# Kernel tuning notes

Measured on AMD Instinct MI355X. Metric: run time of the kernel, lower is better.

## Reference

```python
import jax, jax.numpy as jnp
import numpy as np

COUNT = 8  # hardcoded 8x8 patch grid in the original module


def setup_inputs() -> dict:
    key = jax.random.key(0)
    kx, = jax.random.split(key, 1)
    x = jax.random.normal(kx, (8, 64, 512, 512), dtype=jnp.float32)
    gamma = jnp.zeros((1,), dtype=jnp.float32)  # nn.Parameter(torch.zeros(1))
    return {"x": x, "gamma": gamma}


def reference(x, gamma):
    B, C, H, W = x.shape
    s = H // COUNT  # stride; original uses height-derived stride for both dims
    # Extract the 8x8 grid of patches without loops:
    # (B,C,H,W) -> (B,C,cnt,s,cnt,s) -> (B,cnt,cnt,C,s,s) -> (B,P,C,s*s)
    p = x.reshape(B, C, COUNT, s, COUNT, s)
    p = p.transpose(0, 2, 4, 1, 3, 5).reshape(B, COUNT * COUNT, C, s * s)
    # channel-channel energy per patch: [B,P,C,C]
    energy = jnp.einsum('bpci,bpdi->bpcd', p, p)
    # DANet trick: max - energy, then softmax over last dim
    energy_new = jnp.max(energy, axis=-1, keepdims=True) - energy
    attention = jax.nn.softmax(energy_new, axis=-1)
    out = jnp.einsum('bpcd,bpdi->bpci', attention, p)
    # reassemble spatial map
    out = out.reshape(B, COUNT, COUNT, C, s, s)
    out = out.transpose(0, 3, 1, 4, 2, 5).reshape(B, C, H, W)
    # NOTE: in the torch code y = x is an alias and x is overwritten in-place,
    # so the final result is gamma * attended + attended.
    return gamma[0] * out + out
```

## Files before the change

### kernel.cpp

```cpp
#include <hip/hip_runtime.h>


#define NW  512
#define HWs 262144

typedef __attribute__((ext_vector_type(4)))  __bf16 bf4;
typedef __attribute__((ext_vector_type(8)))  __bf16 bf8;
typedef __attribute__((ext_vector_type(16))) float  f32x16;

#define MFMA __builtin_amdgcn_mfma_f32_32x32x16_bf16
#define F4E(v,j) ((j)==0?(v).x:(j)==1?(v).y:(j)==2?(v).z:(v).w)

__device__ __forceinline__ void bar_lgkm() {
  asm volatile("s_waitcnt lgkmcnt(0)" ::: "memory");
  __builtin_amdgcn_s_barrier();
}

__device__ __forceinline__ int soff(int c, int rb) {
  return c * 1024 + (rb & 512) + ((rb & 511) ^ ((c & 31) << 4));
}

extern "C" __global__ __launch_bounds__(512, 2)
void k1_gram(const float* __restrict__ x, float* __restrict__ ep) {
  __shared__ char lds[133120];
  char* sHi = lds;
  char* sLo = lds + 65536;
  float* S_lds = (float*)lds;

  const int t   = threadIdx.x;
  const int w8  = t >> 6;
  const int l   = t & 63;
  const int l31 = l & 31, hh = l >> 5;
  const int pc  = w8;
  const int cld = t >> 7;
  const int hf  = (t >> 6) & 1;

  const int bid = blockIdx.x;
  const int b  = bid >> 5;
  const int pr = (bid >> 2) & 7;
  const int hq = bid & 3;
  const float* xb = x + (size_t)b * 64 * HWs + (size_t)(pr * 64 + hq * 16) * NW
                  + hf * 256 + l * 4;

  f32x16 aG00, aG01, aG10, aG11, aS00, aS01, aS10, aS11;
#pragma unroll
  for (int i = 0; i < 16; ++i) {
    aG00[i]=0.f; aG01[i]=0.f; aG10[i]=0.f; aG11[i]=0.f;
    aS00[i]=0.f; aS01[i]=0.f; aS10[i]=0.f; aS11[i]=0.f;
  }

  float4 ra[16];
#pragma unroll
  for (int j = 0; j < 16; ++j)
    ra[j] = *(const float4*)(xb + (size_t)(j * 4 + cld) * HWs);

  for (int r = 0; r < 16; ++r) {
#pragma unroll
    for (int j = 0; j < 16; ++j) {
      const int c = j * 4 + cld;
      const float4 v = ra[j];
      bf4 h, lo;
      h[0]=(__bf16)v.x; h[1]=(__bf16)v.y; h[2]=(__bf16)v.z; h[3]=(__bf16)v.w;
      lo[0]=(__bf16)(v.x-(float)h[0]); lo[1]=(__bf16)(v.y-(float)h[1]);
      lo[2]=(__bf16)(v.z-(float)h[2]); lo[3]=(__bf16)(v.w-(float)h[3]);
      const int wb = c * 1024 + hf * 512 + ((l * 8) ^ ((c & 31) << 4));
      *(bf4*)(sHi + wb) = h;
      *(bf4*)(sLo + wb) = lo;
    }
    if (r + 1 < 16) {
#pragma unroll
      for (int j = 0; j < 16; ++j)
        ra[j] = *(const float4*)(xb + (size_t)(j * 4 + cld) * HWs
                                 + (size_t)(r + 1) * NW);
    }
    bar_lgkm();
#pragma unroll
    for (int ks = 0; ks < 4; ++ks) {
      const int rb = pc * 128 + ks * 32 + hh * 16;
      const bf8 a0 = *(const bf8*)(sHi + soff(l31, rb));
      const bf8 a1 = *(const bf8*)(sHi + soff(32 + l31, rb));
      const bf8 q0 = *(const bf8*)(sLo + soff(l31, rb));
      const bf8 q1 = *(const bf8*)(sLo + soff(32 + l31, rb));
      aG00 = MFMA(a0, a0, aG00, 0, 0, 0);
      aG01 = MFMA(a0, a1, aG01, 0, 0, 0);
      aG10 = MFMA(a1, a0, aG10, 0, 0, 0);
      aG11 = MFMA(a1, a1, aG11, 0, 0, 0);
      aS00 = MFMA(a0, q0, aS00, 0, 0, 0);
      aS01 = MFMA(a0, q1, aS01, 0, 0, 0);
      aS10 = MFMA(a1, q0, aS10, 0, 0, 0);
      aS11 = MFMA(a1, q1, aS11, 0, 0, 0);
    }
    bar_lgkm();
  }

#pragma unroll
  for (int i = 0; i < 16; ++i) {
    const int rr = (i & 3) + ((i >> 2) << 3) + (hh << 2);
    S_lds[pc * 4160 + (rr)      * 65 + l31]      = aS00[i];
    S_lds[pc * 4160 + (rr)      * 65 + 32 + l31] = aS01[i];
    S_lds[pc * 4160 + (32 + rr) * 65 + l31]      = aS10[i];
    S_lds[pc * 4160 + (32 + rr) * 65 + 32 + l31] = aS11[i];
  }
  bar_lgkm();
  const int pat = b * 64 + pr * 8 + pc;
  float* epb = ep + ((size_t)(pat * 4 + hq) << 12);
#pragma unroll
  for (int i = 0; i < 16; ++i) {
    const int rr = (i & 3) + ((i >> 2) << 3) + (hh << 2);
    epb[(rr)      * 64 + l31]      = aG00[i] + aS00[i] + S_lds[pc*4160 + (l31)    *65 + rr];
    epb[(rr)      * 64 + 32 + l31] = aG01[i] + aS01[i] + S_lds[pc*4160 + (32+l31) *65 + rr];
    epb[(32 + rr) * 64 + l31]      = aG10[i] + aS10[i] + S_lds[pc*4160 + (l31)    *65 + 32 + rr];
    epb[(32 + rr) * 64 + 32 + l31] = aG11[i] + aS11[i] + S_lds[pc*4160 + (32+l31) *65 + 32 + rr];
  }
}

extern "C" __global__ __launch_bounds__(256)
void k2_softmax(const float* __restrict__ ep, const float* __restrict__ g,
                __bf16* __restrict__ attn) {
  const int pat = blockIdx.x;
  const int w4 = threadIdx.x >> 6, l = threadIdx.x & 63;
  const float gs = 1.0f + g[0];
  const float* e0 = ep + ((size_t)(pat * 4) << 12);
#pragma unroll 1
  for (int cc = 0; cc < 16; ++cc) {
    const int c = w4 * 16 + cc;
    const int o = c * 64 + l;
    const float e = e0[o] + e0[4096 + o] + e0[8192 + o] + e0[12288 + o];
    float mn = e;
#pragma unroll
    for (int off = 32; off; off >>= 1) mn = fminf(mn, __shfl_xor(mn, off));
    const float w = __expf(mn - e);
    float s = w;
#pragma unroll
    for (int off = 32; off; off >>= 1) s += __shfl_xor(s, off);
    attn[(size_t)pat * 4096 + o] = (__bf16)(gs * w / s);
  }
}

extern "C" __global__ __launch_bounds__(512, 2)
void k3_pv(const float* __restrict__ x, const __bf16* __restrict__ attn,
           float* __restrict__ out) {
  __shared__ char lds[139264];
  char* nat = lds;
  char* pT  = lds + 65536;

  const int t   = threadIdx.x;
  const int w8  = t >> 6;
  const int l   = t & 63;
  const int l31 = l & 31, hh = l >> 5;
  const int pc  = w8;
  const int cld = t >> 7;
  const int hf  = (t >> 6) & 1;
  const int cb  = t & 15;
  const int wb0 = t >> 4;

  const int bid = blockIdx.x;
  const int b  = bid >> 5;
  const int pr = (bid >> 2) & 7;
  const int hq = bid & 3;
  const float* xb = x + (size_t)b * 64 * HWs + (size_t)(pr * 64 + hq * 16) * NW
                  + hf * 256 + l * 4;
  float* ob = out + (size_t)b * 64 * HWs + (size_t)(pr * 64 + hq * 16) * NW;
  const int pat = b * 64 + pr * 8 + pc;

  bf8 af0[4], af1[4];
#pragma unroll
  for (int ks = 0; ks < 4; ++ks) {
    af0[ks] = *(const bf8*)(attn + (size_t)pat * 4096 + (l31)      * 64 + ks * 16 + hh * 8);
    af1[ks] = *(const bf8*)(attn + (size_t)pat * 4096 + (32 + l31) * 64 + ks * 16 + hh * 8);
  }

  float4 ra[16];
#pragma unroll
  for (int j = 0; j < 16; ++j)
    ra[j] = *(const float4*)(xb + (size_t)(j * 4 + cld) * HWs);

  for (int r = 0; r < 16; ++r) {
#pragma unroll
    for (int j = 0; j < 16; ++j) {
      const int c = j * 4 + cld;
      const float4 v = ra[j];
      bf4 h;
      h[0]=(__bf16)v.x; h[1]=(__bf16)v.y; h[2]=(__bf16)v.z; h[3]=(__bf16)v.w;
      *(bf4*)(nat + c * 1024 + hf * 512 + ((l * 8) ^ ((c & 31) << 4))) = h;
    }
    if (r + 1 < 16) {
#pragma unroll
      for (int j = 0; j < 16; ++j)
        ra[j] = *(const float4*)(xb + (size_t)(j * 4 + cld) * HWs
                                 + (size_t)(r + 1) * NW);
    }
    bar_lgkm();
#pragma unroll
    for (int kk = 0; kk < 4; ++kk) {
      const int w0 = (wb0 + kk * 32) * 4;
      bf4 rd0, rd1, rd2, rd3;
      {
        const int c0 = cb * 4;
        const int hfb = (w0 >> 8) * 512;
        const int ib2 = (w0 & 255) * 2;
        rd0 = *(const bf4*)(nat + (c0    ) * 1024 + hfb + (ib2 ^ (((c0    ) & 31) << 4)));
        rd1 = *(const bf4*)(nat + (c0 + 1) * 1024 + hfb + (ib2 ^ (((c0 + 1) & 31) << 4)));
        rd2 = *(const bf4*)(nat + (c0 + 2) * 1024 + hfb + (ib2 ^ (((c0 + 2) & 31) << 4)));
        rd3 = *(const bf4*)(nat + (c0 + 3) * 1024 + hfb + (ib2 ^ (((c0 + 3) & 31) << 4)));
      }
#pragma unroll
      for (int jj = 0; jj < 4; ++jj) {
        bf4 wv;
        wv[0] = rd0[jj]; wv[1] = rd1[jj]; wv[2] = rd2[jj]; wv[3] = rd3[jj];
        *(bf4*)(pT + (size_t)(w0 + jj) * 144 + cb * 8) = wv;
      }
    }
    bar_lgkm();
#pragma unroll
    for (int ib = 0; ib < 2; ++ib) {
      f32x16 o0, o1;
#pragma unroll
      for (int i = 0; i < 16; ++i) { o0[i] = 0.f; o1[i] = 0.f; }
      const char* prow = pT + (size_t)(pc * 64 + ib * 32 + l31) * 144;
#pragma unroll
      for (int ks = 0; ks < 4; ++ks) {
        const bf8 pa = *(const bf8*)(prow + ks * 32 + hh * 16);
        o0 = MFMA(pa, af0[ks], o0, 0, 0, 0);
        o1 = MFMA(pa, af1[ks], o1, 0, 0, 0);
      }
#pragma unroll
      for (int rq = 0; rq < 4; ++rq) {
        const int wloc = pc * 64 + ib * 32 + rq * 8 + hh * 4;
        float* orow = ob + (size_t)r * NW + wloc;
        float4 q0; q0.x=o0[rq*4+0]; q0.y=o0[rq*4+1]; q0.z=o0[rq*4+2]; q0.w=o0[rq*4+3];
        *(float4*)(orow + (size_t)l31 * HWs) = q0;
        float4 q1; q1.x=o1[rq*4+0]; q1.y=o1[rq*4+1]; q1.z=o1[rq*4+2]; q1.w=o1[rq*4+3];
        *(float4*)(orow + (size_t)(32 + l31) * HWs) = q1;
      }
    }
    bar_lgkm();
  }
}

#define NS1 16
#define NS3 16

__device__ __forceinline__ void fb_load1(const float* g1, int st, float4 (&R)[16]) {
  const float* gp = g1 + (size_t)st * 4 * NW;
#pragma unroll
  for (int rl = 0; rl < 4; ++rl)
#pragma unroll
    for (int j = 0; j < 4; ++j)
      R[rl * 4 + j] = *(const float4*)(gp + (size_t)rl * NW + j * 4);
}
__device__ __forceinline__ void fb_cvtw1(char* wH, char* wL, int q_ld, int swzw,
                                         const float4 (&R)[16]) {
#pragma unroll
  for (int rl = 0; rl < 4; ++rl)
#pragma unroll
    for (int s = 0; s < 2; ++s) {
      const float4 va = R[rl * 4 + s * 2], vb = R[rl * 4 + s * 2 + 1];
      const float f[8] = {va.x, va.y, va.z, va.w, vb.x, vb.y, vb.z, vb.w};
      bf8 h, lo;
#pragma unroll
      for (int e = 0; e < 8; ++e) { h[e] = (__bf16)f[e]; lo[e] = (__bf16)(f[e] - (float)h[e]); }
      const int boff = (rl * 128 + q_ld * 32 + s * 16) ^ swzw;
      *(bf8*)(wH + boff) = h;
      *(bf8*)(wL + boff) = lo;
    }
}
__device__ __forceinline__ void fb_load3(const float* g3, int st, float4 (&R)[16]) {
  const float* gp = g3 + (size_t)st * 4 * NW;
#pragma unroll
  for (int cc = 0; cc < 4; ++cc)
#pragma unroll
    for (int j = 0; j < 4; ++j)
      R[cc * 4 + j] = *(const float4*)(gp + (size_t)cc * HWs + j * 4);
}
__device__ __forceinline__ void fb_cvtw3(char* sT, int cg, int iq, const float4 (&R)[16]) {
#pragma unroll
  for (int w = 0; w < 16; ++w) {
    bf4 q;
#pragma unroll
    for (int cc = 0; cc < 4; ++cc) q[cc] = (__bf16)F4E(R[cc * 4 + (w >> 2)], w & 3);
    const int iloc = iq * 16 + w;
    const int sw = ((iloc & 15) ^ ((iloc >> 4) & 7)) << 4;
    const int boff = (iloc & 127) * 256 + ((((iloc >> 7) << 7) + cg * 8) ^ sw);
    *(bf4*)(sT + boff) = q;
  }
}
extern "C" __global__ __launch_bounds__(256, 2)
void spectralAgg_fallback(const float* __restrict__ x, const float* __restrict__ g,
                          float* __restrict__ out) {
  __shared__ char lds[73728];
  char* sH = lds;
  char* sL = lds + 32768;
  char* sA = lds + 65536;
  const int t = threadIdx.x, wv = t >> 6, l = t & 63, l31 = l & 31, hh = l >> 5;
  const int wg = blockIdx.x, b = wg >> 6, pp = wg & 63, pr = pp >> 3, pcq = pp & 7;
  const size_t pbase = (size_t)b*64*HWs + (size_t)(pr*64)*NW + (size_t)(pcq*64);
  const float* xp = x + pbase;
  float* op = out + pbase;
  const int c_ld = t >> 2, q_ld = t & 3;
  const float* g1 = xp + (size_t)c_ld * HWs + q_ld * 16;
  char* wH = sH + c_ld * 512;
  char* wL = sL + c_ld * 512;
  const int swzw = (c_ld & 31) << 4;
  const int ct = wv >> 1, dt = wv & 1;
  const char* pA  = sH + (size_t)(ct*32+l31)*512;
  const char* pBh = sH + (size_t)(dt*32+l31)*512;
  const char* pBl = sL + (size_t)(dt*32+l31)*512;
  const int swzr = l31 << 4;
  f32x16 accG, accS;
#pragma unroll
  for (int i = 0; i < 16; ++i) { accG[i] = 0.f; accS[i] = 0.f; }
  float4 ra[16], rb[16];
  fb_load1(g1, 0, ra);
  for (int st = 0; st < NS1; ++st) {
    fb_load1(g1, (st + 1 < NS1) ? st + 1 : st, rb);
    fb_cvtw1(wH, wL, q_ld, swzw, ra);
    bar_lgkm();
#pragma unroll
    for (int k0 = 0; k0 < 16; ++k0) {
      const int off = (k0 * 32 + hh * 16) ^ swzr;
      const bf8 a  = *(const bf8*)(pA + off);
      const bf8 bh = *(const bf8*)(pBh + off);
      const bf8 bl = *(const bf8*)(pBl + off);
      accG = MFMA(a, bh, accG, 0, 0, 0);
      accS = MFMA(a, bl, accS, 0, 0, 0);
    }
    bar_lgkm();
#pragma unroll
    for (int e = 0; e < 16; ++e) ra[e] = rb[e];
  }
  float* S_lds = (float*)sL;
  float* E_lds = (float*)sH;
#pragma unroll
  for (int i = 0; i < 16; ++i) {
    const int cr = ct*32 + (i&3) + ((i>>2)<<3) + (hh<<2);
    S_lds[cr*64 + dt*32 + l31] = accS[i];
  }
  bar_lgkm();
#pragma unroll
  for (int i = 0; i < 16; ++i) {
    const int cr = ct*32 + (i&3) + ((i>>2)<<3) + (hh<<2);
    const int d = dt*32 + l31;
    E_lds[cr*64 + d] = accG[i] + accS[i] + S_lds[d*64 + cr];
  }
  bar_lgkm();
  const int cg = t >> 4, iq = t & 15;
  const float* g3 = xp + (size_t)(cg*4)*HWs + (size_t)(iq>>2)*NW + (iq&3)*16;
  fb_load3(g3, 0, ra);
  const float gs = 1.0f + g[0];
#pragma unroll 1
  for (int rr = 0; rr < 16; ++rr) {
    const int c = wv*16 + rr;
    const float e = E_lds[c*64 + l];
    float mn = e;
#pragma unroll
    for (int o = 32; o; o >>= 1) mn = fminf(mn, __shfl_xor(mn, o));
    const float w = __expf(mn - e);
    float s = w;
#pragma unroll
    for (int o = 32; o; o >>= 1) s += __shfl_xor(s, o);
    *(__bf16*)(sA + c*128 + ((l*2) ^ ((c&7)<<4))) = (__bf16)(gs * w / s);
  }
  bar_lgkm();
  bf8 bfr[2][4];
#pragma unroll
  for (int c2 = 0; c2 < 2; ++c2)
#pragma unroll
    for (int k0 = 0; k0 < 4; ++k0)
      bfr[c2][k0] = *(const bf8*)(sA + (size_t)(c2*32+l31)*128 +
                                  ((k0*32 + hh*16) ^ ((l31&7)<<4)));
  for (int st = 0; st < NS3; ++st) {
    fb_load3(g3, (st + 1 < NS3) ? st + 1 : st, rb);
    fb_cvtw3(sH, cg, iq, ra);
    bar_lgkm();
    f32x16 oo0[2], oo1[2];
#pragma unroll
    for (int it = 0; it < 2; ++it)
#pragma unroll
      for (int i = 0; i < 16; ++i) { oo0[it][i] = 0.f; oo1[it][i] = 0.f; }
#pragma unroll
    for (int it = 0; it < 2; ++it) {
      const int i = wv*64 + it*32 + l31;
      const char* base = sH + (size_t)(i & 127) * 256;
      const int hb = (i >> 7) * 128;
      const int sw = ((i & 15) ^ ((i >> 4) & 7)) << 4;
#pragma unroll
      for (int k0 = 0; k0 < 4; ++k0) {
        const bf8 pa = *(const bf8*)(base + ((hb + k0*32 + hh*16) ^ sw));
        oo0[it] = MFMA(pa, bfr[0][k0], oo0[it], 0, 0, 0);
        oo1[it] = MFMA(pa, bfr[1][k0], oo1[it], 0, 0, 0);
      }
    }
#pragma unroll
    for (int it = 0; it < 2; ++it)
#pragma unroll
      for (int rq = 0; rq < 4; ++rq) {
        const int iloc = wv*64 + it*32 + rq*8 + hh*4;
        const int gi = st*256 + iloc;
        float* oprow = op + (size_t)(gi >> 6)*NW + (gi & 63);
        float4 q0; q0.x=oo0[it][rq*4+0]; q0.y=oo0[it][rq*4+1]; q0.z=oo0[it][rq*4+2]; q0.w=oo0[it][rq*4+3];
        *(float4*)(oprow + (size_t)l31*HWs) = q0;
        float4 q1; q1.x=oo1[it][rq*4+0]; q1.y=oo1[it][rq*4+1]; q1.z=oo1[it][rq*4+2]; q1.w=oo1[it][rq*4+3];
        *(float4*)(oprow + (size_t)(32+l31)*HWs) = q1;
      }
    bar_lgkm();
#pragma unroll
    for (int e = 0; e < 16; ++e) ra[e] = rb[e];
  }
}

extern "C" void kernel_launch(void* const* d_in, const int* in_sizes, int n_in,
                              void* d_out, int out_size, void* d_ws, size_t ws_size,
                              hipStream_t stream) {
  const float* x = (const float*)d_in[0];
  const float* g = (const float*)d_in[1];
  float* o = (float*)d_out;
  const size_t need = (size_t)512 * 4 * 4096 * 4 + (size_t)512 * 4096 * 2;
  if (ws_size >= need) {
    float* ep = (float*)d_ws;
    __bf16* attn = (__bf16*)((char*)d_ws + (size_t)512 * 4 * 4096 * 4);
    k1_gram<<<dim3(256), dim3(512), 0, stream>>>(x, ep);
    k2_softmax<<<dim3(512), dim3(256), 0, stream>>>(ep, g, attn);
    k3_pv<<<dim3(256), dim3(512), 0, stream>>>(x, attn, o);
  } else {
    spectralAgg_fallback<<<dim3(512), dim3(256), 0, stream>>>(x, g, o);
  }
}
```

Before: 412.5 us.

## Stage bf16 patch-major copy of x in gram kernel for reuse by PV kernel

The gram kernel now also writes a bf16, patch-major, channel-interleaved copy of x to workspace, so the PV kernel reads half the bytes and skips its in-LDS transpose. The gram kernel is split across twice as many blocks, each covering half the width with a 32-channel tile per wave, which halves LDS use. The PV kernel is restructured to loop over patches with double-buffered swizzled LDS tiles. This adds an extra 256 MB global write in k1 and a larger workspace requirement, in exchange for cheaper k3 loads.

```diff
diff --git a/kernel.cpp b/kernel.cpp
--- a/kernel.cpp
+++ b/kernel.cpp
@@ -16,101 +16,108 @@
   __builtin_amdgcn_s_barrier();
 }
 
-__device__ __forceinline__ int soff(int c, int rb) {
-  return c * 1024 + (rb & 512) + ((rb & 511) ^ ((c & 31) << 4));
-}
-
-extern "C" __global__ __launch_bounds__(512, 2)
-void k1_gram(const float* __restrict__ x, float* __restrict__ ep) {
-  __shared__ char lds[133120];
+extern "C" __global__ __launch_bounds__(512)
+void k1_gram(const float* __restrict__ x, float* __restrict__ ep,
+             __bf16* __restrict__ wsHi) {
+  __shared__ char lds[66560];
   char* sHi = lds;
-  char* sLo = lds + 65536;
+  char* sLo = lds + 32768;
   float* S_lds = (float*)lds;
 
-  const int t   = threadIdx.x;
-  const int w8  = t >> 6;
-  const int l   = t & 63;
-  const int l31 = l & 31, hh = l >> 5;
-  const int pc  = w8;
-  const int cld = t >> 7;
-  const int hf  = (t >> 6) & 1;
+  const int T   = threadIdx.x;
+  const int wv8 = T >> 6;
+  const int l   = T & 63;
+  const int l31 = l & 31;
+  const int hh  = l >> 5;
 
   const int bid = blockIdx.x;
-  const int b  = bid >> 5;
-  const int pr = (bid >> 2) & 7;
-  const int hq = bid & 3;
-  const float* xb = x + (size_t)b * 64 * HWs + (size_t)(pr * 64 + hq * 16) * NW
-                  + hf * 256 + l * 4;
-
-  f32x16 aG00, aG01, aG10, aG11, aS00, aS01, aS10, aS11;
-#pragma unroll
-  for (int i = 0; i < 16; ++i) {
-    aG00[i]=0.f; aG01[i]=0.f; aG10[i]=0.f; aG11[i]=0.f;
-    aS00[i]=0.f; aS01[i]=0.f; aS10[i]=0.f; aS11[i]=0.f;
-  }
-
-  float4 ra[16];
-#pragma unroll
-  for (int j = 0; j < 16; ++j)
-    ra[j] = *(const float4*)(xb + (size_t)(j * 4 + cld) * HWs);
+  const int wh = bid & 1;
+  const int hq = (bid >> 1) & 3;
+  const int pr = (bid >> 3) & 7;
+  const int b  = bid >> 6;
+
+  const int pl = wv8 & 3;
+  const int ct = wv8 >> 2;
+  const int pc = wh * 4 + pl;
+  const int pat  = b * 64 + pr * 8 + pc;
+  const int row0 = pr * 64 + hq * 16;
+
+  const float* xb = x + (size_t)b * 64 * HWs + (size_t)row0 * NW + wh * 256 + l * 4;
+
+  f32x16 G0, G1, S0, S1;
+#pragma unroll
+  for (int i = 0; i < 16; ++i) { G0[i]=0.f; G1[i]=0.f; S0[i]=0.f; S1[i]=0.f; }
+
+  float4 rA[8], rB[8];
+#pragma unroll
+  for (int j = 0; j < 8; ++j)
+    rA[j] = *(const float4*)(xb + (size_t)(wv8 * 8 + j) * HWs);
 
   for (int r = 0; r < 16; ++r) {
-#pragma unroll
-    for (int j = 0; j < 16; ++j) {
-      const int c = j * 4 + cld;
-      const float4 v = ra[j];
+    if (r + 1 < 16) {
+#pragma unroll
+      for (int j = 0; j < 8; ++j)
+        rB[j] = *(const float4*)(xb + (size_t)(wv8 * 8 + j) * HWs + (size_t)(r + 1) * NW);
+    }
+    bf4 hA[8];
+#pragma unroll
+    for (int j = 0; j < 8; ++j) {
+      const int c = wv8 * 8 + j;
+      const float4 v = rA[j];
       bf4 h, lo;
       h[0]=(__bf16)v.x; h[1]=(__bf16)v.y; h[2]=(__bf16)v.z; h[3]=(__bf16)v.w;
       lo[0]=(__bf16)(v.x-(float)h[0]); lo[1]=(__bf16)(v.y-(float)h[1]);
       lo[2]=(__bf16)(v.z-(float)h[2]); lo[3]=(__bf16)(v.w-(float)h[3]);
-      const int wb = c * 1024 + hf * 512 + ((l * 8) ^ ((c & 31) << 4));
-      *(bf4*)(sHi + wb) = h;
-      *(bf4*)(sLo + wb) = lo;
-    }
-    if (r + 1 < 16) {
-#pragma unroll
-      for (int j = 0; j < 16; ++j)
-        ra[j] = *(const float4*)(xb + (size_t)(j * 4 + cld) * HWs
-                                 + (size_t)(r + 1) * NW);
+      hA[j] = h;
+      const int off = c * 512 + ((l * 8) ^ ((c & 31) << 4));
+      *(bf4*)(sHi + off) = h;
+      *(bf4*)(sLo + off) = lo;
+    }
+#pragma unroll
+    for (int k2 = 0; k2 < 4; ++k2) {
+      bf8 pk;
+#pragma unroll
+      for (int jj = 0; jj < 8; ++jj) pk[jj] = hA[jj][k2];
+      const int wloc256 = l * 4 + k2;
+      const int pl_w = wloc256 >> 6;
+      const int w_loc = wloc256 & 63;
+      const int pat_w = b * 64 + pr * 8 + wh * 4 + pl_w;
+      const int i = (hq * 16 + r) * 64 + w_loc;
+      *(bf8*)((char*)wsHi + (size_t)pat_w * 524288 + (size_t)i * 128 + wv8 * 16) = pk;
     }
     bar_lgkm();
 #pragma unroll
     for (int ks = 0; ks < 4; ++ks) {
-      const int rb = pc * 128 + ks * 32 + hh * 16;
-      const bf8 a0 = *(const bf8*)(sHi + soff(l31, rb));
-      const bf8 a1 = *(const bf8*)(sHi + soff(32 + l31, rb));
-      const bf8 q0 = *(const bf8*)(sLo + soff(l31, rb));
-      const bf8 q1 = *(const bf8*)(sLo + soff(32 + l31, rb));
-      aG00 = MFMA(a0, a0, aG00, 0, 0, 0);
-      aG01 = MFMA(a0, a1, aG01, 0, 0, 0);
-      aG10 = MFMA(a1, a0, aG10, 0, 0, 0);
-      aG11 = MFMA(a1, a1, aG11, 0, 0, 0);
-      aS00 = MFMA(a0, q0, aS00, 0, 0, 0);
-      aS01 = MFMA(a0, q1, aS01, 0, 0, 0);
-      aS10 = MFMA(a1, q0, aS10, 0, 0, 0);
-      aS11 = MFMA(a1, q1, aS11, 0, 0, 0);
-    }
-    bar_lgkm();
+      const int kb = pl * 128 + ks * 32 + hh * 16;
+      const int ca = ct * 32 + l31;
+      const bf8 a   = *(const bf8*)(sHi + ca * 512 + (kb ^ ((ca & 31) << 4)));
+      const bf8 bh0 = *(const bf8*)(sHi + l31 * 512 + (kb ^ ((l31 & 31) << 4)));
+      const bf8 bh1 = *(const bf8*)(sHi + (32 + l31) * 512 + (kb ^ (((32 + l31) & 31) << 4)));
+      const bf8 bl0 = *(const bf8*)(sLo + l31 * 512 + (kb ^ ((l31 & 31) << 4)));
+      const bf8 bl1 = *(const bf8*)(sLo + (32 + l31) * 512 + (kb ^ (((32 + l31) & 31) << 4)));
+      G0 = MFMA(a, bh0, G0, 0, 0, 0);
+      G1 = MFMA(a, bh1, G1, 0, 0, 0);
+      S0 = MFMA(a, bl0, S0, 0, 0, 0);
+      S1 = MFMA(a, bl1, S1, 0, 0, 0);
+    }
+    bar_lgkm();
+#pragma unroll
+    for (int e = 0; e < 8; ++e) rA[e] = rB[e];
   }
 
 #pragma unroll
   for (int i = 0; i < 16; ++i) {
-    const int rr = (i & 3) + ((i >> 2) << 3) + (hh << 2);
-    S_lds[pc * 4160 + (rr)      * 65 + l31]      = aS00[i];
-    S_lds[pc * 4160 + (rr)      * 65 + 32 + l31] = aS01[i];
-    S_lds[pc * 4160 + (32 + rr) * 65 + l31]      = aS10[i];
-    S_lds[pc * 4160 + (32 + rr) * 65 + 32 + l31] = aS11[i];
+    const int cr = ct * 32 + (i & 3) + ((i >> 2) << 3) + (hh << 2);
+    S_lds[pl * 4160 + cr * 65 + l31]      = S0[i];
+    S_lds[pl * 4160 + cr * 65 + 32 + l31] = S1[i];
   }
   bar_lgkm();
-  const int pat = b * 64 + pr * 8 + pc;
   float* epb = ep + ((size_t)(pat * 4 + hq) << 12);
 #pragma unroll
   for (int i = 0; i < 16; ++i) {
-    const int rr = (i & 3) + ((i >> 2) << 3) + (hh << 2);
-    epb[(rr)      * 64 + l31]      = aG00[i] + aS00[i] + S_lds[pc*4160 + (l31)    *65 + rr];
-    epb[(rr)      * 64 + 32 + l31] = aG01[i] + aS01[i] + S_lds[pc*4160 + (32+l31) *65 + rr];
-    epb[(32 + rr) * 64 + l31]      = aG10[i] + aS10[i] + S_lds[pc*4160 + (l31)    *65 + 32 + rr];
-    epb[(32 + rr) * 64 + 32 + l31] = aG11[i] + aS11[i] + S_lds[pc*4160 + (32+l31) *65 + 32 + rr];
+    const int cr = ct * 32 + (i & 3) + ((i >> 2) << 3) + (hh << 2);
+    epb[cr * 64 + l31]      = G0[i] + S0[i] + S_lds[pl * 4160 + l31 * 65 + cr];
+    epb[cr * 64 + 32 + l31] = G1[i] + S1[i] + S_lds[pl * 4160 + (32 + l31) * 65 + cr];
   }
 }
 
@@ -137,110 +144,91 @@
   }
 }
 
-extern "C" __global__ __launch_bounds__(512, 2)
-void k3_pv(const float* __restrict__ x, const __bf16* __restrict__ attn,
+extern "C" __global__ __launch_bounds__(512)
+void k3_pv(const __bf16* __restrict__ wsHi, const __bf16* __restrict__ attn,
            float* __restrict__ out) {
-  __shared__ char lds[139264];
-  char* nat = lds;
-  char* pT  = lds + 65536;
-
-  const int t   = threadIdx.x;
-  const int w8  = t >> 6;
-  const int l   = t & 63;
-  const int l31 = l & 31, hh = l >> 5;
-  const int pc  = w8;
-  const int cld = t >> 7;
-  const int hf  = (t >> 6) & 1;
-  const int cb  = t & 15;
-  const int wb0 = t >> 4;
+  __shared__ char lds[65536];
+  const int T   = threadIdx.x;
+  const int wv8 = T >> 6;
+  const int l   = T & 63;
+  const int l31 = l & 31;
+  const int hh  = l >> 5;
 
   const int bid = blockIdx.x;
+  const int hq = bid & 3;
+  const int pr = (bid >> 2) & 7;
   const int b  = bid >> 5;
-  const int pr = (bid >> 2) & 7;
-  const int hq = bid & 3;
-  const float* xb = x + (size_t)b * 64 * HWs + (size_t)(pr * 64 + hq * 16) * NW
-                  + hf * 256 + l * 4;
-  float* ob = out + (size_t)b * 64 * HWs + (size_t)(pr * 64 + hq * 16) * NW;
-  const int pat = b * 64 + pr * 8 + pc;
-
-  bf8 af0[4], af1[4];
-#pragma unroll
-  for (int ks = 0; ks < 4; ++ks) {
-    af0[ks] = *(const bf8*)(attn + (size_t)pat * 4096 + (l31)      * 64 + ks * 16 + hh * 8);
-    af1[ks] = *(const bf8*)(attn + (size_t)pat * 4096 + (32 + l31) * 64 + ks * 16 + hh * 8);
-  }
-
-  float4 ra[16];
-#pragma unroll
-  for (int j = 0; j < 16; ++j)
-    ra[j] = *(const float4*)(xb + (size_t)(j * 4 + cld) * HWs);
-
-  for (int r = 0; r < 16; ++r) {
-#pragma unroll
-    for (int j = 0; j < 16; ++j) {
-      const int c = j * 4 + cld;
-      const float4 v = ra[j];
-      bf4 h;
-      h[0]=(__bf16)v.x; h[1]=(__bf16)v.y; h[2]=(__bf16)v.z; h[3]=(__bf16)v.w;
-      *(bf4*)(nat + c * 1024 + hf * 512 + ((l * 8) ^ ((c & 31) << 4))) = h;
-    }
-    if (r + 1 < 16) {
-#pragma unroll
-      for (int j = 0; j < 16; ++j)
-        ra[j] = *(const float4*)(xb + (size_t)(j * 4 + cld) * HWs
-                                 + (size_t)(r + 1) * NW);
-    }
-    bar_lgkm();
-#pragma unroll
-    for (int kk = 0; kk < 4; ++kk) {
-      const int w0 = (wb0 + kk * 32) * 4;
-      bf4 rd0, rd1, rd2, rd3;
-      {
-        const int c0 = cb * 4;
-        const int hfb = (w0 >> 8) * 512;
-        const int ib2 = (w0 & 255) * 2;
-        rd0 = *(const bf4*)(nat + (c0    ) * 1024 + hfb + (ib2 ^ (((c0    ) & 31) << 4)));
-        rd1 = *(const bf4*)(nat + (c0 + 1) * 1024 + hfb + (ib2 ^ (((c0 + 1) & 31) << 4)));
-        rd2 = *(const bf4*)(nat + (c0 + 2) * 1024 + hfb + (ib2 ^ (((c0 + 2) & 31) << 4)));
-        rd3 = *(const bf4*)(nat + (c0 + 3) * 1024 + hfb + (ib2 ^ (((c0 + 3) & 31) << 4)));
-      }
-#pragma unroll
-      for (int jj = 0; jj < 4; ++jj) {
-        bf4 wv;
-        wv[0] = rd0[jj]; wv[1] = rd1[jj]; wv[2] = rd2[jj]; wv[3] = rd3[jj];
-        *(bf4*)(pT + (size_t)(w0 + jj) * 144 + cb * 8) = wv;
-      }
-    }
-    bar_lgkm();
-#pragma unroll
-    for (int ib = 0; ib < 2; ++ib) {
+
+  const int ii  = T >> 1;
+  const int haf = T & 1;
+
+  float4 rS[4], rT[4];
+  {
+    const size_t src0 = (size_t)(b * 64 + pr * 8) * 524288 + (size_t)(hq * 1024) * 128;
+#pragma unroll
+    for (int q = 0; q < 4; ++q)
+      rS[q] = *(const float4*)((const char*)wsHi + src0 + (size_t)ii * 128 + haf * 64 + q * 16);
+  }
+
+  for (int p = 0; p < 8; ++p) {
+    const int pat = b * 64 + pr * 8 + p;
+    bf8 af[2][4];
+#pragma unroll
+    for (int mt = 0; mt < 2; ++mt)
+#pragma unroll
+      for (int ks = 0; ks < 4; ++ks)
+        af[mt][ks] = *(const bf8*)(attn + (size_t)pat * 4096 +
+                                   (mt * 32 + l31) * 64 + ks * 16 + hh * 8);
+
+    for (int cc = 0; cc < 4; ++cc) {
+      const int s = p * 4 + cc;
+      char* buf = lds + (s & 1) * 32768;
+#pragma unroll
+      for (int q = 0; q < 4; ++q) {
+        const int off = ii * 128 + (((haf * 64 + q * 16)) ^ ((ii & 7) << 4));
+        *(float4*)(buf + off) = rS[q];
+      }
+      if (s + 1 < 32) {
+        const int pn = (s + 1) >> 2, cn = (s + 1) & 3;
+        const size_t src = (size_t)(b * 64 + pr * 8 + pn) * 524288 +
+                           (size_t)(hq * 1024 + cn * 256) * 128;
+#pragma unroll
+        for (int q = 0; q < 4; ++q)
+          rT[q] = *(const float4*)((const char*)wsHi + src + (size_t)ii * 128 + haf * 64 + q * 16);
+      }
+      bar_lgkm();
+
       f32x16 o0, o1;
 #pragma unroll
       for (int i = 0; i < 16; ++i) { o0[i] = 0.f; o1[i] = 0.f; }
-      const char* prow = pT + (size_t)(pc * 64 + ib * 32 + l31) * 144;
 #pragma unroll
       for (int ks = 0; ks < 4; ++ks) {
-        const bf8 pa = *(const bf8*)(prow + ks * 32 + hh * 16);
-        o0 = MFMA(pa, af0[ks], o0, 0, 0, 0);
-        o1 = MFMA(pa, af1[ks], o1, 0, 0, 0);
-      }
+        const int irow = wv8 * 32 + l31;
+        const bf8 pa = *(const bf8*)(buf + irow * 128 +
+                                     (((ks * 32 + hh * 16)) ^ ((irow & 7) << 4)));
+        o0 = MFMA(pa, af[0][ks], o0, 0, 0, 0);
+        o1 = MFMA(pa, af[1][ks], o1, 0, 0, 0);
+      }
+      const int i_base = hq * 1024 + cc * 256 + wv8 * 32;
 #pragma unroll
       for (int rq = 0; rq < 4; ++rq) {
-        const int wloc = pc * 64 + ib * 32 + rq * 8 + hh * 4;
-        float* orow = ob + (size_t)r * NW + wloc;
+        const int ig = i_base + rq * 8 + hh * 4;
+        const int rl = ig >> 6, wl = ig & 63;
+        float* orow = out + (size_t)b * 64 * HWs + (size_t)(pr * 64 + rl) * NW + p * 64 + wl;
         float4 q0; q0.x=o0[rq*4+0]; q0.y=o0[rq*4+1]; q0.z=o0[rq*4+2]; q0.w=o0[rq*4+3];
         *(float4*)(orow + (size_t)l31 * HWs) = q0;
         float4 q1; q1.x=o1[rq*4+0]; q1.y=o1[rq*4+1]; q1.z=o1[rq*4+2]; q1.w=o1[rq*4+3];
         *(float4*)(orow + (size_t)(32 + l31) * HWs) = q1;
       }
-    }
-    bar_lgkm();
+      bar_lgkm();
+#pragma unroll
+      for (int e = 0; e < 4; ++e) rS[e] = rT[e];
+    }
   }
 }
 
 #define NS1 16
 #define NS3 16
-
 __device__ __forceinline__ void fb_load1(const float* g1, int st, float4 (&R)[16]) {
   const float* gp = g1 + (size_t)st * 4 * NW;
 #pragma unroll
@@ -415,13 +403,16 @@
   const float* x = (const float*)d_in[0];
   const float* g = (const float*)d_in[1];
   float* o = (float*)d_out;
-  const size_t need = (size_t)512 * 4 * 4096 * 4 + (size_t)512 * 4096 * 2;
-  if (ws_size >= need) {
-    float* ep = (float*)d_ws;
-    __bf16* attn = (__bf16*)((char*)d_ws + (size_t)512 * 4 * 4096 * 4);
-    k1_gram<<<dim3(256), dim3(512), 0, stream>>>(x, ep);
+  const size_t epB  = (size_t)512 * 4 * 4096 * 4;
+  const size_t aB   = (size_t)512 * 4096 * 2;
+  const size_t hiB  = (size_t)512 * 524288;
+  if (ws_size >= epB + aB + hiB) {
+    float*  ep   = (float*)d_ws;
+    __bf16* attn = (__bf16*)((char*)d_ws + epB);
+    __bf16* wsHi = (__bf16*)((char*)d_ws + epB + aB);
+    k1_gram<<<dim3(512), dim3(512), 0, stream>>>(x, ep, wsHi);
     k2_softmax<<<dim3(512), dim3(256), 0, stream>>>(ep, g, attn);
-    k3_pv<<<dim3(256), dim3(512), 0, stream>>>(x, attn, o);
+    k3_pv<<<dim3(256), dim3(512), 0, stream>>>(wsHi, attn, o);
   } else {
     spectralAgg_fallback<<<dim3(512), dim3(256), 0, stream>>>(x, g, o);
   }
```

Result: no change. 410.8 us (-0.4%).
